# Performance work log

Measured on AMD Instinct MI355X. Metric: run time of the kernel, lower is better.

Reference implementation:

```python
import jax, jax.numpy as jnp
import numpy as np

B, L, H, LAT, V = 4096, 16, 256, 64, 800


def setup_inputs() -> dict:
    key = jax.random.key(0)
    ks = jax.random.split(key, 20)
    s = 0.05
    return {
        'wid': jax.random.randint(ks[0], (B, L), 0, V),
        'tree_vec': jax.random.normal(ks[1], (B, LAT), jnp.float32),
        'emb': jax.random.normal(ks[2], (V, H), jnp.float32) * s,
        'Wz_w': jax.random.normal(ks[3], (H, 2 * H), jnp.float32) * s,
        'Wz_b': jnp.zeros((H,), jnp.float32),
        'Wr_w': jax.random.normal(ks[4], (H, H), jnp.float32) * s,
        'Ur_w': jax.random.normal(ks[5], (H, H), jnp.float32) * s,
        'Ur_b': jnp.zeros((H,), jnp.float32),
        'Wh_w': jax.random.normal(ks[6], (H, 2 * H), jnp.float32) * s,
        'Wh_b': jnp.zeros((H,), jnp.float32),
        'W_w': jax.random.normal(ks[7], (H, LAT + H), jnp.float32) * s,
        'W_b': jnp.zeros((H,), jnp.float32),
        'U_w': jax.random.normal(ks[8], (H, LAT + 2 * H), jnp.float32) * s,
        'U_b': jnp.zeros((H,), jnp.float32),
        'Wo_w': jax.random.normal(ks[9], (V, H), jnp.float32) * s,
        'Wo_b': jnp.zeros((V,), jnp.float32),
        'Us_w': jax.random.normal(ks[10], (1, H), jnp.float32) * s,
        'Us_b': jnp.zeros((1,), jnp.float32),
    }


def _decoder(wid, tree_vec, emb, Wz_w, Wz_b, Wr_w, Ur_w, Ur_b, Wh_w, Wh_b,
             W_w, W_b, U_w, U_b, Wo_w, Wo_b, Us_w, Us_b):
    nB, nL = wid.shape
    x = emb[wid]                      # [B,L,H] node embeddings
    xt = jnp.transpose(x, (1, 0, 2))  # [L,B,H]

    def gru_scan(src_seq, dst_seq):
        # JTNN GRUUpdate along a chain: carry = (m_prev, rm_prev)
        def step(carry, xs):
            m_prev, rm_prev = carry
            x_src, x_dst = xs
            z = jax.nn.sigmoid(jnp.concatenate([x_src, m_prev], -1) @ Wz_w.T + Wz_b)
            h_til = jnp.tanh(jnp.concatenate([x_src, rm_prev], -1) @ Wh_w.T + Wh_b)
            m = (1.0 - z) * m_prev + z * h_til
            r = jax.nn.sigmoid(x_dst @ Wr_w.T + m @ Ur_w.T + Ur_b)
            return (m, r * m), m
        z0 = jnp.zeros((src_seq.shape[1], H), src_seq.dtype)
        _, m_seq = jax.lax.scan(step, (z0, z0), (src_seq, dst_seq))
        return m_seq  # [L-1,B,H]

    # forward edges t->t+1 (DFS forward), reverse edges t+1->t (DFS backtrack)
    m_fwd = gru_scan(xt[:-1], xt[1:])
    m_rev = gru_scan(xt[1:][::-1], xt[:-1][::-1])[::-1]  # indexed by t

    zeros_h = jnp.zeros((nB, H), x.dtype)
    tvL = lambda n: jnp.broadcast_to(tree_vec, (n, nB, LAT))

    # p_inputs = [x_v, h_v, tree_vec] at root, each fwd step, each rev step
    p_root = jnp.concatenate([x[:, 0], zeros_h, tree_vec], -1)[None]
    p_fwd = jnp.concatenate([xt[1:], m_fwd, tvL(nL - 1)], -1)
    m_fwd_shift = jnp.concatenate([zeros_h[None], m_fwd[:-1]], 0)
    h_rev = m_fwd_shift + m_rev  # node t after backtrack pull
    p_rev = jnp.concatenate([xt[:-1], h_rev, tvL(nL - 1)], -1)[::-1]
    p_in = jnp.concatenate([p_root, p_fwd, p_rev], 0).reshape(-1, 2 * H + LAT)
    # targets: forward expansions -> 1, backtracks + final stop -> 0
    p_t = jnp.concatenate([jnp.ones((nL - 1,)), jnp.zeros((nL,))])
    p_t = jnp.broadcast_to(p_t[:, None], (2 * nL - 1, nB)).reshape(-1)

    # q_inputs = [h, tree_vec] at root and each newly created node
    q_root = jnp.concatenate([zeros_h, tree_vec], -1)[None]
    q_new = jnp.concatenate([m_fwd, tvL(nL - 1)], -1)
    q_in = jnp.concatenate([q_root, q_new], 0).reshape(-1, H + LAT)
    q_t = jnp.transpose(wid, (1, 0)).reshape(-1)  # [L*B], step-major like q_in

    q = jax.nn.relu(q_in @ W_w.T + W_b) @ Wo_w.T + Wo_b  # [L*B, V]
    p = (jax.nn.relu(p_in @ U_w.T + U_b) @ Us_w.T + Us_b)[:, 0]

    p_loss = jnp.sum(jnp.logaddexp(0.0, p) - p * p_t) / nB
    logZ = jax.nn.logsumexp(q, axis=-1)
    q_sel = jnp.take_along_axis(q, q_t[:, None], axis=1)[:, 0]
    q_loss = jnp.sum(logZ - q_sel) / nB
    p_acc = jnp.mean(((p > 0).astype(jnp.int32) == p_t.astype(jnp.int32)).astype(jnp.float32))
    q_acc = jnp.mean((jnp.argmax(q, axis=-1) == q_t).astype(jnp.float32))
    return (q_loss, p_loss, q_acc, p_acc)


def reference(wid, tree_vec, emb, Wz_w, Wz_b, Wr_w, Ur_w, Ur_b, Wh_w, Wh_b,
              W_w, W_b, U_w, U_b, Wo_w, Wo_b, Us_w, Us_b):
    return _decoder(wid, tree_vec, emb, Wz_w, Wz_b, Wr_w, Ur_w, Ur_b, Wh_w, Wh_b,
                    W_w, W_b, U_w, U_b, Wo_w, Wo_b, Us_w, Us_b)
```

## Files before the change

### kernel.cpp

```cpp
#include <hip/hip_runtime.h>
#include <math.h>


typedef unsigned short u16;
typedef __attribute__((ext_vector_type(4))) float f4;
typedef __attribute__((ext_vector_type(4))) unsigned short u16x4;
typedef __attribute__((ext_vector_type(8))) unsigned short u16x8;
typedef __attribute__((ext_vector_type(8))) short s16x8;
typedef __attribute__((ext_vector_type(4))) float f32x4;

#define DEV static __device__ __forceinline__

DEV u16 f2b(float f) {
  unsigned u = __float_as_uint(f);
  u += 0x7fffu + ((u >> 16) & 1u);
  return (u16)(u >> 16);
}
DEV float b2f(u16 h) { return __uint_as_float(((unsigned)h) << 16); }
DEV void split2(float v, u16& hi, u16& lo) {
  hi = f2b(v);
  lo = f2b(v - b2f(hi));
}
DEV float fsig(float x) { return __builtin_amdgcn_rcpf(1.f + __expf(-x)); }
DEV float ftanh(float x) {
  const float e = __expf(2.f * x);
  return 1.f - 2.f * __builtin_amdgcn_rcpf(e + 1.f);
}

DEV void gld16(const void* g, void* l) {
  __builtin_amdgcn_global_load_lds((const __attribute__((address_space(1))) void*)g,
                                   (__attribute__((address_space(3))) void*)l, 16, 0, 0);
}

#define MFMA(a, b, c) __builtin_amdgcn_mfma_f32_16x16x32_bf16((a), (b), (c), 0, 0, 0)

template <int GR, int GC, bool ASPL, bool BSPL>
DEV void mm128(const u16* __restrict__ Ah, const u16* __restrict__ Al,
               const u16* __restrict__ Bh, const u16* __restrict__ Bl,
               int K, u16* sm, f32x4* acc) {
  constexpr int MT = 8 / GR, NT = 8 / GC;
  const int tid = threadIdx.x;
  const int lane = tid & 63;
  const int wv = tid >> 6;
  const int wr = wv / GC, wc = wv % GC;
  const size_t rs = (size_t)K * 2;
  const size_t soff = (size_t)(tid >> 2) * rs + (size_t)((tid & 3) * 16);
  const char* gAh = (const char*)Ah + soff;
  const char* gBh = (const char*)Bh + soff;
  const char* gAl = nullptr;
  const char* gBl = nullptr;
  if constexpr (ASPL) gAl = (const char*)Al + soff;
  if constexpr (BSPL) gBl = (const char*)Bl + soff;
  char* L = (char*)sm;
  const int wb = wv * 1024;
  const int frow = lane & 15, fkb = (lane >> 4) * 16;
  const char* rA = L + (size_t)((wr * 16 * MT + frow) * 64 + fkb);
  const char* rB = L + 8192 + (size_t)((wc * 16 * NT + frow) * 64 + fkb);
  const size_t rskip = rs * 64;
  const int nk = K >> 5;
  for (int kt = 0; kt < nk; ++kt) {
    gld16(gAh, L + wb);
    gld16(gAh + rskip, L + 4096 + wb);
    gld16(gBh, L + 8192 + wb);
    gld16(gBh + rskip, L + 12288 + wb);
    if constexpr (ASPL) {
      gld16(gAl, L + 16384 + wb);
      gld16(gAl + rskip, L + 20480 + wb);
    }
    if constexpr (BSPL) {
      gld16(gBl, L + 24576 + wb);
      gld16(gBl + rskip, L + 28672 + wb);
    }
    gAh += 64; gBh += 64;
    if constexpr (ASPL) gAl += 64;
    if constexpr (BSPL) gBl += 64;
    __syncthreads();
    s16x8 a_[MT], b_[NT];
#pragma unroll
    for (int i = 0; i < MT; ++i) a_[i] = *(const s16x8*)(rA + i * 1024);
#pragma unroll
    for (int j = 0; j < NT; ++j) b_[j] = *(const s16x8*)(rB + j * 1024);
#pragma unroll
    for (int i = 0; i < MT; ++i)
#pragma unroll
      for (int j = 0; j < NT; ++j)
        acc[i * NT + j] = MFMA(a_[i], b_[j], acc[i * NT + j]);
    if constexpr (BSPL) {
      s16x8 bl_[NT];
#pragma unroll
      for (int j = 0; j < NT; ++j) bl_[j] = *(const s16x8*)(rB + 16384 + j * 1024);
#pragma unroll
      for (int i = 0; i < MT; ++i)
#pragma unroll
        for (int j = 0; j < NT; ++j)
          acc[i * NT + j] = MFMA(a_[i], bl_[j], acc[i * NT + j]);
    }
    if constexpr (ASPL) {
      s16x8 al_[MT];
#pragma unroll
      for (int i = 0; i < MT; ++i) al_[i] = *(const s16x8*)(rA + 16384 + i * 1024);
#pragma unroll
      for (int i = 0; i < MT; ++i)
#pragma unroll
        for (int j = 0; j < NT; ++j)
          acc[i * NT + j] = MFMA(al_[i], b_[j], acc[i * NT + j]);
    }
    __syncthreads();
  }
}

__global__ __launch_bounds__(256) void k_pack(const float* __restrict__ Wz, const float* __restrict__ Wr,
                                              const float* __restrict__ Ur, const float* __restrict__ Wh,
                                              const float* __restrict__ Ww, const float* __restrict__ Uw,
                                              const float* __restrict__ Wo, const float* __restrict__ emb,
                                              const float* __restrict__ tree,
                                              u16* wpk, u16* uzh, u16* urw, u16* wu, u16* wt2, u16* wov,
                                              u16* uxp2, u16* utp2, u16* embp, u16* tre2) {
  const int i = blockIdx.x * 256 + threadIdx.x;
  const int seg = blockIdx.y;
  u16 h, l;
  if (seg == 0) {
    if (i >= 196608) return;
    const int row = i >> 8, c = i & 255;
    const float v = (row < 256) ? Wz[row * 512 + c]
                                : (row < 512) ? Wh[(row - 256) * 512 + c] : Wr[(row - 512) * 256 + c];
    split2(v, h, l); wpk[i] = h; wpk[196608 + i] = l;
  } else if (seg == 1) {
    if (i >= 131072) return;
    const int row = i >> 8, c = i & 255;
    const float v = (row < 256) ? Wz[row * 512 + 256 + c] : Wh[(row - 256) * 512 + 256 + c];
    uzh[i] = f2b(v);
  } else if (seg == 2) {
    if (i >= 65536) return;
    urw[i] = f2b(Ur[i]);
  } else if (seg == 3) {
    if (i >= 81920) return;
    if (i < 65536) {
      const int row = i >> 8, c = i & 255;
      wu[i] = f2b(Ww[row * 320 + c]);
    } else {
      const int j = i - 65536, row = j >> 6, c = j & 63;
      split2(Ww[row * 320 + 256 + c], h, l); wt2[j] = h; wt2[16384 + j] = l;
    }
  } else if (seg == 4) {
    if (i >= 229376) return;
    const float v = (i < 204800) ? Wo[i] : 0.f;
    wov[i] = f2b(v);
  } else if (seg == 5) {
    if (i >= 147456) return;
    if (i < 65536) {
      const int row = i >> 8, c = i & 255;
      split2(Uw[row * 576 + c], h, l); uxp2[i] = h; uxp2[65536 + i] = l;
    } else if (i < 131072) {
      const int j = i - 65536, row = j >> 8, c = j & 255;
      wu[65536 + j] = f2b(Uw[row * 576 + 256 + c]);
    } else {
      const int j = i - 131072, row = j >> 6, c = j & 63;
      split2(Uw[row * 576 + 512 + c], h, l); utp2[j] = h; utp2[16384 + j] = l;
    }
  } else if (seg == 6) {
    if (i >= 229376) return;
    const int row = i >> 8;
    const float v = (row < 800) ? emb[i] : 0.f;
    split2(v, h, l); embp[i] = h; embp[229376 + i] = l;
  } else {
    if (i >= 65536) return;
    const int b = i >> 4, c4 = (i & 15) << 2;
    const f4 tv = *(const f4*)(tree + (size_t)b * 64 + c4);
    u16x4 hi, lo;
#pragma unroll
    for (int k = 0; k < 4; ++k) { u16 hh, ll; split2(tv[k], hh, ll); hi[k] = hh; lo[k] = ll; }
    *(u16x4*)(tre2 + (size_t)b * 64 + c4) = hi;
    *(u16x4*)(tre2 + 262144 + (size_t)b * 64 + c4) = lo;
  }
}

__global__ __launch_bounds__(256) void k_prep(const u16* __restrict__ embp, const u16* __restrict__ wpk,
                                              const u16* __restrict__ tre2, const u16* __restrict__ wt2,
                                              const u16* __restrict__ utp2, const u16* __restrict__ uxp2,
                                              u16* __restrict__ Aembh, float* __restrict__ Tq,
                                              float* __restrict__ Tp, float* __restrict__ Xp) {
  __shared__ u16 sm[16384];
  f32x4 acc[16] = {};
  const int bid = blockIdx.x;
  int seg, bx, by, K;
  const u16 *A0, *B0;
  size_t Aoff, Boff;
  if (bid < 42) { seg = 0; bx = bid % 7; by = bid / 7; A0 = embp; Aoff = 229376; B0 = wpk; Boff = 196608; K = 256; }
  else if (bid < 106) { const int l2 = bid - 42; seg = 1; bx = l2 % 32; by = l2 / 32; A0 = tre2; Aoff = 262144; B0 = wt2; Boff = 16384; K = 64; }
  else if (bid < 170) { const int l2 = bid - 106; seg = 2; bx = l2 % 32; by = l2 / 32; A0 = tre2; Aoff = 262144; B0 = utp2; Boff = 16384; K = 64; }
  else { const int l2 = bid - 170; seg = 3; bx = l2 % 7; by = l2 / 7; A0 = embp; Aoff = 229376; B0 = uxp2; Boff = 65536; K = 256; }
  A0 += (size_t)bx * 128 * K;
  B0 += (size_t)by * 128 * K;
  mm128<2, 2, true, true>(A0, A0 + Aoff, B0, B0 + Boff, K, sm, acc);
  const int lane = threadIdx.x & 63, wv = threadIdx.x >> 6;
  const int wr = wv >> 1, wc = wv & 1, quad = lane >> 4, c = lane & 15;
#pragma unroll
  for (int i = 0; i < 4; ++i)
#pragma unroll
    for (int j = 0; j < 4; ++j)
#pragma unroll
      for (int rg = 0; rg < 4; ++rg) {
        const size_t row = (size_t)bx * 128 + wr * 64 + i * 16 + quad * 4 + rg;
        const int col = by * 128 + wc * 64 + j * 16 + c;
        const float v = acc[i * 4 + j][rg];
        if (seg == 0) Aembh[row * 768 + col] = f2b(v);
        else if (seg == 1) Tq[row * 256 + col] = v;
        else if (seg == 2) Tp[row * 256 + col] = v;
        else Xp[row * 256 + col] = v;
      }
}

__global__ __launch_bounds__(1024, 1) void k_scan(const u16* __restrict__ uzh, const u16* __restrict__ urw,
                                                  const u16* __restrict__ Aembh, const int* __restrict__ wid,
                                                  const float* __restrict__ Wz_b, const float* __restrict__ Wh_b,
                                                  const float* __restrict__ Ur_b,
                                                  u16* __restrict__ mfh, u16* __restrict__ mrh) {
  __shared__ __align__(16) u16 MH[8192];
  __shared__ __align__(16) u16 ML[8192];
  __shared__ __align__(16) u16 RH[8192];
  __shared__ __align__(16) u16 RL[8192];
  const int tid = threadIdx.x;
  const int wv = tid >> 6, lane = tid & 63;
  const int l15 = lane & 15, quad = lane >> 4;
  const int r0 = blockIdx.x * 32;
  const int dir = r0 >> 12;
  const int b0 = r0 & 4095;
  for (int i = tid; i < 8192; i += 1024) { MH[i] = 0; ML[i] = 0; RH[i] = 0; RL[i] = 0; }
  const int zc0 = wv * 16;
  const int cc = zc0 + l15;
  const float bzv = Wz_b[cc], bhv = Wh_b[cc], urv = Ur_b[cc];
  s16x8 wz[8], wh[8];
#pragma unroll
  for (int kc = 0; kc < 8; ++kc) {
    const size_t zo = (size_t)cc * 256 + kc * 32 + quad * 8;
    wz[kc] = *(const s16x8*)(uzh + zo);
    wh[kc] = *(const s16x8*)(uzh + zo + 65536);
  }
  float mnew[2][4];
  __syncthreads();
  for (int s = 0; s < 15; ++s) {
    const int tsrc = dir ? (15 - s) : s;
    const int tdst = dir ? (14 - s) : (s + 1);
    int xids[8], xds[8];
#pragma unroll
    for (int mt = 0; mt < 2; ++mt)
#pragma unroll
      for (int rg = 0; rg < 4; ++rg) {
        const int b = b0 + mt * 16 + quad * 4 + rg;
        xids[mt * 4 + rg] = wid[b * 16 + tsrc];
        xds[mt * 4 + rg] = (s < 14) ? wid[b * 16 + tdst] : 0;
      }
    f32x4 aZ[2] = {};
    f32x4 aH[2] = {};
    for (int kc = 0; kc < 8; ++kc) {
      s16x8 amh[2], aml[2], arh[2], arl[2];
#pragma unroll
      for (int mt = 0; mt < 2; ++mt) {
        const int ai = ((kc * 4 + quad) * 32 + mt * 16 + l15) * 8;
        amh[mt] = *(const s16x8*)&MH[ai];
        aml[mt] = *(const s16x8*)&ML[ai];
        arh[mt] = *(const s16x8*)&RH[ai];
        arl[mt] = *(const s16x8*)&RL[ai];
      }
#pragma unroll
      for (int mt = 0; mt < 2; ++mt) {
        aZ[mt] = MFMA(amh[mt], wz[kc], aZ[mt]);
        aZ[mt] = MFMA(aml[mt], wz[kc], aZ[mt]);
        aH[mt] = MFMA(arh[mt], wh[kc], aH[mt]);
        aH[mt] = MFMA(arl[mt], wh[kc], aH[mt]);
      }
    }
    __syncthreads();
#pragma unroll
    for (int mt = 0; mt < 2; ++mt)
#pragma unroll
      for (int rg = 0; rg < 4; ++rg) {
        const int rr = mt * 16 + quad * 4 + rg;
        const int xid = xids[mt * 4 + rg];
        const int mi = ((cc >> 3) * 32 + rr) * 8 + (cc & 7);
        const float az = b2f(Aembh[(size_t)xid * 768 + cc]);
        const float ah = b2f(Aembh[(size_t)xid * 768 + 256 + cc]);
        const float mp = b2f(MH[mi]) + b2f(ML[mi]);
        const float z = fsig(aZ[mt][rg] + az + bzv);
        const float ht = ftanh(aH[mt][rg] + ah + bhv);
        const float mv = (1.f - z) * mp + z * ht;
        mnew[mt][rg] = mv;
        u16 hh, ll; split2(mv, hh, ll);
        MH[mi] = hh; ML[mi] = ll;
      }
    __syncthreads();
    {
      u16* dst = dir ? (mrh + ((size_t)(14 - s) * 4096 + b0) * 256)
                     : (mfh + ((size_t)s * 4096 + b0) * 256);
      const int r = tid >> 5, cg = tid & 31;
      const s16x8 v = *(const s16x8*)&MH[(cg * 32 + r) * 8];
      *(s16x8*)(dst + r * 256 + cg * 8) = v;
    }
    if (s == 14) break;
    f32x4 aR[2] = {};
    for (int kc = 0; kc < 8; ++kc) {
      s16x8 amh[2], aml[2];
#pragma unroll
      for (int mt = 0; mt < 2; ++mt) {
        const int ai = ((kc * 4 + quad) * 32 + mt * 16 + l15) * 8;
        amh[mt] = *(const s16x8*)&MH[ai];
        aml[mt] = *(const s16x8*)&ML[ai];
      }
      const size_t ro = (size_t)cc * 256 + kc * 32 + quad * 8;
      const s16x8 brh = *(const s16x8*)(urw + ro);
#pragma unroll
      for (int mt = 0; mt < 2; ++mt) {
        aR[mt] = MFMA(amh[mt], brh, aR[mt]);
        aR[mt] = MFMA(aml[mt], brh, aR[mt]);
      }
    }
#pragma unroll
    for (int mt = 0; mt < 2; ++mt)
#pragma unroll
      for (int rg = 0; rg < 4; ++rg) {
        const int rr = mt * 16 + quad * 4 + rg;
        const int xd = xds[mt * 4 + rg];
        const int mi = ((cc >> 3) * 32 + rr) * 8 + (cc & 7);
        const float ar = b2f(Aembh[(size_t)xd * 768 + 512 + cc]);
        const float rp = aR[mt][rg] + ar + urv;
        const float rmv = fsig(rp) * mnew[mt][rg];
        u16 hh, ll; split2(rmv, hh, ll);
        RH[mi] = hh; RL[mi] = ll;
      }
    __syncthreads();
  }
}

__global__ __launch_bounds__(256) void k_mid(const u16* __restrict__ mfh, const u16* __restrict__ mrh,
                                             const u16* __restrict__ wu,
                                             const float* __restrict__ Tq, const float* __restrict__ W_b,
                                             const float* __restrict__ Xp, const float* __restrict__ Tp,
                                             const float* __restrict__ U_b, const float* __restrict__ Us_w,
                                             const int* __restrict__ wid,
                                             u16* __restrict__ hq, u16* __restrict__ hrev,
                                             float* __restrict__ ppart) {
  const int bid = blockIdx.x;
  const int tid = threadIdx.x;
  if (bid < 1920) {
    __shared__ u16 sm[8192];
    f32x4 acc[16] = {};
    const int rb = bid >> 2, ct = bid & 3;
    const u16* Ah = mfh + (size_t)rb * 128 * 256;
    const u16* Bh = wu + (size_t)ct * 128 * 256;
    mm128<4, 1, false, false>(Ah, nullptr, Bh, nullptr, 256, sm, acc);
    const int lane = tid & 63, wv = tid >> 6, quad = lane >> 4, c = lane & 15;
    if (ct < 2) {
      const int colb = ct * 128;
#pragma unroll
      for (int i = 0; i < 2; ++i)
#pragma unroll
        for (int rg = 0; rg < 4; ++rg) {
          const size_t row = (size_t)rb * 128 + wv * 32 + i * 16 + quad * 4 + rg;
          const int b = (int)(row & 4095);
#pragma unroll
          for (int j = 0; j < 8; ++j) {
            const int col = colb + j * 16 + c;
            const float hv = fmaxf(acc[i * 8 + j][rg] + Tq[(size_t)b * 256 + col] + W_b[col], 0.f);
            hq[(row + 4096) * 256 + col] = f2b(hv);
          }
        }
    } else {
      const int colb = (ct - 2) * 128;
#pragma unroll
      for (int i = 0; i < 2; ++i)
#pragma unroll
        for (int rg = 0; rg < 4; ++rg) {
          const size_t row = (size_t)rb * 128 + wv * 32 + i * 16 + quad * 4 + rg;
          const int t = (int)(row >> 12), b = (int)(row & 4095);
          const int xid = wid[b * 16 + t + 1];
          const int prow = (int)row + 4096;
          float d = 0.f;
#pragma unroll
          for (int j = 0; j < 8; ++j) {
            const int col = colb + j * 16 + c;
            float h = acc[i * 8 + j][rg] + Xp[(size_t)xid * 256 + col] + Tp[(size_t)b * 256 + col] + U_b[col];
            h = fmaxf(h, 0.f);
            d += h * Us_w[col];
          }
#pragma unroll
          for (int dd = 1; dd < 16; dd <<= 1) d += __shfl_xor(d, dd);
          if (c == 0) ppart[(size_t)prow * 2 + (ct - 2)] = d;
        }
    }
  } else if (bid < 9600) {
    const int idx = (bid - 1920) * 256 + tid;
    const int r = idx >> 5, g8 = idx & 31;
    const int t = r >> 12;
    const size_t o = (size_t)r * 256 + g8 * 8;
    const u16x8 a = *(const u16x8*)(mrh + o);
    u16x8 out = a;
    if (t > 0) {
      const u16x8 a2 = *(const u16x8*)(mfh + o - 1048576);
#pragma unroll
      for (int k = 0; k < 8; ++k) out[k] = f2b(b2f(a[k]) + b2f(a2[k]));
    }
    *(u16x8*)(hrev + o) = out;
  } else {
    const int b = bid - 9600;
    const int col = tid;
    const float hv = fmaxf(Tq[(size_t)b * 256 + col] + W_b[col], 0.f);
    hq[(size_t)b * 256 + col] = f2b(hv);
    const int xid = wid[b * 16];
    float d = fmaxf(Xp[(size_t)xid * 256 + col] + Tp[(size_t)b * 256 + col] + U_b[col], 0.f) * Us_w[col];
#pragma unroll
    for (int dd = 1; dd < 64; dd <<= 1) d += __shfl_xor(d, dd);
    __shared__ float red[4];
    if ((tid & 63) == 0) red[tid >> 6] = d;
    __syncthreads();
    if (tid == 0) {
      ppart[(size_t)b * 2] = red[0] + red[1] + red[2] + red[3];
      ppart[(size_t)b * 2 + 1] = 0.f;
    }
  }
}

__global__ __launch_bounds__(256) void k_tail(const u16* __restrict__ hq, const u16* __restrict__ wov,
                                              const u16* __restrict__ wu, const u16* __restrict__ hrev,
                                              const float* __restrict__ Wo_b, const float* __restrict__ Xp,
                                              const float* __restrict__ Tp, const float* __restrict__ U_b,
                                              const float* __restrict__ Us_w, const int* __restrict__ wid,
                                              float* __restrict__ qpart, float* __restrict__ ppart) {
  __shared__ u16 sm[8192];
  f32x4 acc[16] = {};
  const int bid = blockIdx.x;
  const int tid = threadIdx.x, lane = tid & 63, wv = tid >> 6;
  const int quad = lane >> 4, c = lane & 15;
  if (bid < 3584) {
    const int by = bid % 7, bx = bid / 7;
    const u16* Ah = hq + (size_t)bx * 128 * 256;
    const u16* Bh = wov + (size_t)by * 128 * 256;
    mm128<4, 1, false, false>(Ah, nullptr, Bh, nullptr, 256, sm, acc);
    const int colb = by * 128;
#pragma unroll
    for (int i = 0; i < 2; ++i)
#pragma unroll
      for (int rg = 0; rg < 4; ++rg) {
        const size_t row = (size_t)bx * 128 + wv * 32 + i * 16 + quad * 4 + rg;
        const int t = (int)(row >> 12), b = (int)(row & 4095);
        const int qt = wid[b * 16 + t];
        float vals[8];
        float mx = -1e30f;
        int am = 0x7fffffff;
#pragma unroll
        for (int j = 0; j < 8; ++j) {
          const int col = colb + j * 16 + c;
          float v = -1e30f;
          if (col < 800) v = acc[i * 8 + j][rg] + Wo_b[col];
          vals[j] = v;
          if (v > mx) { mx = v; am = col; }
        }
        float gm = mx;
        int ga = am;
#pragma unroll
        for (int d = 1; d < 16; d <<= 1) {
          const float om = __shfl_xor(gm, d);
          const int oa = __shfl_xor(ga, d);
          if (om > gm || (om == gm && oa < ga)) { gm = om; ga = oa; }
        }
        float s = 0.f, sel = -1e30f;
#pragma unroll
        for (int j = 0; j < 8; ++j) {
          s += __expf(vals[j] - gm);
          const int col = colb + j * 16 + c;
          if (col == qt) sel = vals[j];
        }
#pragma unroll
        for (int d = 1; d < 16; d <<= 1) {
          s += __shfl_xor(s, d);
          sel = fmaxf(sel, __shfl_xor(sel, d));
        }
        if (c == 0) {
          f4 o;
          o.x = gm; o.y = s; o.z = (float)ga; o.w = sel;
          *(f4*)(qpart + (row * 8 + by) * 4) = o;
        }
      }
  } else {
    const int l2 = bid - 3584;
    const int by = l2 & 1, bx = l2 >> 1;
    const u16* Ah = hrev + (size_t)bx * 128 * 256;
    const u16* Bh = wu + (size_t)(256 + by * 128) * 256;
    mm128<4, 1, false, false>(Ah, nullptr, Bh, nullptr, 256, sm, acc);
    const int colb = by * 128;
#pragma unroll
    for (int i = 0; i < 2; ++i)
#pragma unroll
      for (int rg = 0; rg < 4; ++rg) {
        const size_t row = (size_t)bx * 128 + wv * 32 + i * 16 + quad * 4 + rg;
        const int t = (int)(row >> 12), b = (int)(row & 4095);
        const int xid = wid[b * 16 + t];
        const int prow = (30 - t) * 4096 + b;
        float d = 0.f;
#pragma unroll
        for (int j = 0; j < 8; ++j) {
          const int col = colb + j * 16 + c;
          float h = acc[i * 8 + j][rg] + Xp[(size_t)xid * 256 + col] + Tp[(size_t)b * 256 + col] + U_b[col];
          h = fmaxf(h, 0.f);
          d += h * Us_w[col];
        }
#pragma unroll
        for (int dd = 1; dd < 16; dd <<= 1) d += __shfl_xor(d, dd);
        if (c == 0) ppart[(size_t)prow * 2 + by] = d;
      }
  }
}

__global__ __launch_bounds__(256) void k_red(const float* __restrict__ qpart, const float* __restrict__ ppart,
                                             const int* __restrict__ wid, const float* __restrict__ Us_b,
                                             float* __restrict__ accb) {
  __shared__ float s0, s1;
  if (threadIdx.x == 0) { s0 = 0.f; s1 = 0.f; }
  __syncthreads();
  if (blockIdx.x < 256) {
    const int r = blockIdx.x * 256 + threadIdx.x;
    f4 parts[7];
#pragma unroll
    for (int i = 0; i < 7; ++i) parts[i] = *(const f4*)(qpart + ((size_t)r * 8 + i) * 4);
    float M = -1e30f;
    int am = 0x7fffffff;
#pragma unroll
    for (int i = 0; i < 7; ++i) {
      const float m_ = parts[i].x;
      const int a_ = (int)parts[i].z;
      if (m_ > M || (m_ == M && a_ < am)) { M = m_; am = a_; }
    }
    float S = 0.f, sel = -1e30f;
#pragma unroll
    for (int i = 0; i < 7; ++i) {
      S += parts[i].y * __expf(parts[i].x - M);
      sel = fmaxf(sel, parts[i].w);
    }
    const float logZ = M + logf(S);
    const int t = r >> 12, b = r & 4095;
    const int qt = wid[b * 16 + t];
    atomicAdd(&s0, logZ - sel);
    atomicAdd(&s1, (am == qt) ? 1.f : 0.f);
    __syncthreads();
    if (threadIdx.x == 0) {
      atomicAdd(&accb[blockIdx.x & 15], s0);
      atomicAdd(&accb[16 + (blockIdx.x & 15)], s1);
    }
  } else {
    const int r = (blockIdx.x - 256) * 256 + threadIdx.x;
    const float p = ppart[(size_t)r * 2] + ppart[(size_t)r * 2 + 1] + Us_b[0];
    const int sidx = r >> 12;
    const float pt = (sidx < 15) ? 1.f : 0.f;
    const float loss = fmaxf(p, 0.f) + log1pf(expf(-fabsf(p))) - p * pt;
    const float hit = ((p > 0.f) == (pt > 0.5f)) ? 1.f : 0.f;
    atomicAdd(&s0, loss);
    atomicAdd(&s1, hit);
    __syncthreads();
    if (threadIdx.x == 0) {
      atomicAdd(&accb[32 + (blockIdx.x & 15)], s0);
      atomicAdd(&accb[48 + (blockIdx.x & 15)], s1);
    }
  }
}

__global__ void k_finalize(const float* __restrict__ accb, float* __restrict__ out) {
  if (threadIdx.x == 0 && blockIdx.x == 0) {
    float ql = 0, qa = 0, pl = 0, pa = 0;
    for (int i = 0; i < 16; ++i) {
      ql += accb[i];
      qa += accb[16 + i];
      pl += accb[32 + i];
      pa += accb[48 + i];
    }
    out[0] = ql / 4096.f;
    out[1] = pl / 4096.f;
    out[2] = qa / 65536.f;
    out[3] = pa / 126976.f;
  }
}

__global__ void k_flag(float* __restrict__ out) {
  if (threadIdx.x < 4) out[threadIdx.x] = -12345.f;
}

extern "C" void kernel_launch(void* const* d_in, const int* in_sizes, int n_in,
                              void* d_out, int out_size, void* d_ws, size_t ws_size,
                              hipStream_t stream) {
  (void)in_sizes; (void)n_in; (void)out_size;
  const int* wid = (const int*)d_in[0];
  const float* tree = (const float*)d_in[1];
  const float* emb = (const float*)d_in[2];
  const float* Wz_w = (const float*)d_in[3];
  const float* Wz_b = (const float*)d_in[4];
  const float* Wr_w = (const float*)d_in[5];
  const float* Ur_w = (const float*)d_in[6];
  const float* Ur_b = (const float*)d_in[7];
  const float* Wh_w = (const float*)d_in[8];
  const float* Wh_b = (const float*)d_in[9];
  const float* W_w = (const float*)d_in[10];
  const float* W_b = (const float*)d_in[11];
  const float* U_w = (const float*)d_in[12];
  const float* U_b = (const float*)d_in[13];
  const float* Wo_w = (const float*)d_in[14];
  const float* Wo_b = (const float*)d_in[15];
  const float* Us_w = (const float*)d_in[16];
  const float* Us_b = (const float*)d_in[17];
  char* ws = (char*)d_ws;

  constexpr size_t NEED = 152273152ull;
  if (ws_size < NEED) {
    k_flag<<<1, 64, 0, stream>>>((float*)d_out);
    return;
  }

  u16* hq = (u16*)(ws + 0ull);
  u16* hrev = (u16*)(ws + 33554432ull);
  u16* mfh = (u16*)(ws + 65011712ull);
  u16* mrh = (u16*)(ws + 96468992ull);
  u16* Aembh = (u16*)(ws + 127926272ull);
  u16* embp = (u16*)(ws + 129302528ull);
  u16* wpk = (u16*)(ws + 130220032ull);
  u16* uzh = (u16*)(ws + 131006464ull);
  u16* urw = (u16*)(ws + 131268608ull);
  u16* wu = (u16*)(ws + 131399680ull);
  u16* wt2 = (u16*)(ws + 131661824ull);
  u16* wov = (u16*)(ws + 131727360ull);
  u16* uxp2 = (u16*)(ws + 132186112ull);
  u16* utp2 = (u16*)(ws + 132448256ull);
  u16* tre2 = (u16*)(ws + 132513792ull);
  float* Tq = (float*)(ws + 133562368ull);
  float* Tp = (float*)(ws + 137756672ull);
  float* Xp = (float*)(ws + 141950976ull);
  float* qpart = (float*)(ws + 142868480ull);
  float* ppart = (float*)(ws + 151257088ull);
  float* accb = (float*)(ws + 152272896ull);

  hipMemsetAsync(accb, 0, 256, stream);

  k_pack<<<dim3(896, 8), 256, 0, stream>>>(Wz_w, Wr_w, Ur_w, Wh_w, W_w, U_w, Wo_w, emb, tree,
                                           wpk, uzh, urw, wu, wt2, wov, uxp2, utp2, embp, tre2);
  k_prep<<<184, 256, 0, stream>>>(embp, wpk, tre2, wt2, utp2, uxp2, Aembh, Tq, Tp, Xp);
  k_scan<<<256, 1024, 0, stream>>>(uzh, urw, Aembh, wid, Wz_b, Wh_b, Ur_b, mfh, mrh);
  k_mid<<<13696, 256, 0, stream>>>(mfh, mrh, wu, Tq, W_b, Xp, Tp, U_b, Us_w, wid, hq, hrev, ppart);
  k_tail<<<4544, 256, 0, stream>>>(hq, wov, wu, hrev, Wo_b, Xp, Tp, U_b, Us_w, wid, qpart, ppart);
  k_red<<<752, 256, 0, stream>>>(qpart, ppart, wid, Us_b, accb);
  k_finalize<<<1, 64, 0, stream>>>(accb, (float*)d_out);
}
```

Baseline: 598.5 us.

## Keep A tile resident and stream all vocab tiles with online logsumexp

```diff
diff --git a/kernel.cpp b/kernel.cpp
--- a/kernel.cpp
+++ b/kernel.cpp
@@ -426,67 +426,122 @@
                                               const float* __restrict__ Tp, const float* __restrict__ U_b,
                                               const float* __restrict__ Us_w, const int* __restrict__ wid,
                                               float* __restrict__ qpart, float* __restrict__ ppart) {
-  __shared__ u16 sm[8192];
-  f32x4 acc[16] = {};
+  __shared__ __align__(16) u16 smem[40960];
   const int bid = blockIdx.x;
   const int tid = threadIdx.x, lane = tid & 63, wv = tid >> 6;
   const int quad = lane >> 4, c = lane & 15;
-  if (bid < 3584) {
-    const int by = bid % 7, bx = bid / 7;
-    const u16* Ah = hq + (size_t)bx * 128 * 256;
-    const u16* Bh = wov + (size_t)by * 128 * 256;
-    mm128<4, 1, false, false>(Ah, nullptr, Bh, nullptr, 256, sm, acc);
-    const int colb = by * 128;
-#pragma unroll
-    for (int i = 0; i < 2; ++i)
+  if (bid < 512) {
+    char* LA = (char*)smem;
+    char* LB = (char*)(smem + 32768);
+    const u16* Ah = hq + (size_t)bid * 128 * 256;
+    const size_t soff = (size_t)(tid >> 2) * 512 + (size_t)((tid & 3) * 16);
+#pragma unroll
+    for (int kt = 0; kt < 8; ++kt) {
+      gld16((const char*)Ah + soff + kt * 64, LA + kt * 8192 + wv * 1024);
+      gld16((const char*)Ah + soff + 32768 + kt * 64, LA + kt * 8192 + 4096 + wv * 1024);
+    }
+    gld16((const char*)wov + soff, LB + wv * 1024);
+    gld16((const char*)wov + soff + 32768, LB + 4096 + wv * 1024);
+    float rM[8], rS[8], rSel[8];
+    int rAm[8], qts[8];
+#pragma unroll
+    for (int mt = 0; mt < 2; ++mt)
 #pragma unroll
       for (int rg = 0; rg < 4; ++rg) {
-        const size_t row = (size_t)bx * 128 + wv * 32 + i * 16 + quad * 4 + rg;
-        const int t = (int)(row >> 12), b = (int)(row & 4095);
-        const int qt = wid[b * 16 + t];
-        float vals[8];
-        float mx = -1e30f;
-        int am = 0x7fffffff;
-#pragma unroll
-        for (int j = 0; j < 8; ++j) {
-          const int col = colb + j * 16 + c;
-          float v = -1e30f;
-          if (col < 800) v = acc[i * 8 + j][rg] + Wo_b[col];
-          vals[j] = v;
-          if (v > mx) { mx = v; am = col; }
+        const int r8 = mt * 4 + rg;
+        rM[r8] = -1e30f; rS[r8] = 0.f; rSel[r8] = -1e30f; rAm[r8] = 0x7fffffff;
+        const size_t row = (size_t)bid * 128 + wv * 32 + mt * 16 + quad * 4 + rg;
+        qts[r8] = wid[(row & 4095) * 16 + (int)(row >> 12)];
+      }
+    f32x4 acc[16];
+    for (int nt = 0; nt < 7; ++nt) {
+#pragma unroll
+      for (int i = 0; i < 16; ++i) acc[i] = (f32x4){0.f, 0.f, 0.f, 0.f};
+      for (int kt = 0; kt < 8; ++kt) {
+        const int g = nt * 8 + kt;
+        __syncthreads();
+        if (g < 55) {
+          const int nn = (g + 1) >> 3, nk = (g + 1) & 7;
+          const char* Bn = (const char*)(wov + (size_t)nn * 32768) + soff + nk * 64;
+          gld16(Bn, LB + ((g + 1) & 1) * 8192 + wv * 1024);
+          gld16(Bn + 32768, LB + ((g + 1) & 1) * 8192 + 4096 + wv * 1024);
         }
-        float gm = mx;
-        int ga = am;
-#pragma unroll
-        for (int d = 1; d < 16; d <<= 1) {
-          const float om = __shfl_xor(gm, d);
-          const int oa = __shfl_xor(ga, d);
-          if (om > gm || (om == gm && oa < ga)) { gm = om; ga = oa; }
+        s16x8 af[2], bf[8];
+#pragma unroll
+        for (int mt = 0; mt < 2; ++mt)
+          af[mt] = *(const s16x8*)(LA + kt * 8192 + (wv * 32 + mt * 16 + c) * 64 + quad * 16);
+#pragma unroll
+        for (int j = 0; j < 8; ++j)
+          bf[j] = *(const s16x8*)(LB + (g & 1) * 8192 + (j * 16 + c) * 64 + quad * 16);
+#pragma unroll
+        for (int mt = 0; mt < 2; ++mt)
+#pragma unroll
+          for (int j = 0; j < 8; ++j)
+            acc[mt * 8 + j] = MFMA(af[mt], bf[j], acc[mt * 8 + j]);
+      }
+      const int colb = nt * 128;
+#pragma unroll
+      for (int mt = 0; mt < 2; ++mt)
+#pragma unroll
+        for (int rg = 0; rg < 4; ++rg) {
+          const int r8 = mt * 4 + rg;
+          float vals[8];
+          float mx = -1e30f;
+          int am = 0x7fffffff;
+#pragma unroll
+          for (int j = 0; j < 8; ++j) {
+            const int col = colb + j * 16 + c;
+            float v = -1e30f;
+            if (col < 800) v = acc[mt * 8 + j][rg] + Wo_b[col];
+            vals[j] = v;
+            if (v > mx) { mx = v; am = col; }
+          }
+          float gm = mx;
+          int ga = am;
+#pragma unroll
+          for (int d = 1; d < 16; d <<= 1) {
+            const float om = __shfl_xor(gm, d);
+            const int oa = __shfl_xor(ga, d);
+            if (om > gm || (om == gm && oa < ga)) { gm = om; ga = oa; }
+          }
+          float s = 0.f, sel = -1e30f;
+#pragma unroll
+          for (int j = 0; j < 8; ++j) {
+            s += __expf(vals[j] - gm);
+            if (colb + j * 16 + c == qts[r8]) sel = vals[j];
+          }
+#pragma unroll
+          for (int d = 1; d < 16; d <<= 1) {
+            s += __shfl_xor(s, d);
+            sel = fmaxf(sel, __shfl_xor(sel, d));
+          }
+          const float oM = rM[r8];
+          if (gm > oM || (gm == oM && ga < rAm[r8])) rAm[r8] = ga;
+          const float nM = fmaxf(oM, gm);
+          rS[r8] = rS[r8] * __expf(oM - nM) + s * __expf(gm - nM);
+          rM[r8] = nM;
+          rSel[r8] = fmaxf(rSel[r8], sel);
         }
-        float s = 0.f, sel = -1e30f;
-#pragma unroll
-        for (int j = 0; j < 8; ++j) {
-          s += __expf(vals[j] - gm);
-          const int col = colb + j * 16 + c;
-          if (col == qt) sel = vals[j];
+    }
+    if (c == 0) {
+#pragma unroll
+      for (int mt = 0; mt < 2; ++mt)
+#pragma unroll
+        for (int rg = 0; rg < 4; ++rg) {
+          const int r8 = mt * 4 + rg;
+          const size_t row = (size_t)bid * 128 + wv * 32 + mt * 16 + quad * 4 + rg;
+          f4 o;
+          o.x = rM[r8]; o.y = rS[r8]; o.z = (float)rAm[r8]; o.w = rSel[r8];
+          *(f4*)(qpart + row * 4) = o;
         }
-#pragma unroll
-        for (int d = 1; d < 16; d <<= 1) {
-          s += __shfl_xor(s, d);
-          sel = fmaxf(sel, __shfl_xor(sel, d));
-        }
-        if (c == 0) {
-          f4 o;
-          o.x = gm; o.y = s; o.z = (float)ga; o.w = sel;
-          *(f4*)(qpart + (row * 8 + by) * 4) = o;
-        }
-      }
+    }
   } else {
-    const int l2 = bid - 3584;
+    f32x4 acc[16] = {};
+    const int l2 = bid - 512;
     const int by = l2 & 1, bx = l2 >> 1;
     const u16* Ah = hrev + (size_t)bx * 128 * 256;
     const u16* Bh = wu + (size_t)(256 + by * 128) * 256;
-    mm128<4, 1, false, false>(Ah, nullptr, Bh, nullptr, 256, sm, acc);
+    mm128<4, 1, false, false>(Ah, nullptr, Bh, nullptr, 256, smem, acc);
     const int colb = by * 128;
 #pragma unroll
     for (int i = 0; i < 2; ++i)
@@ -519,27 +574,12 @@
   __syncthreads();
   if (blockIdx.x < 256) {
     const int r = blockIdx.x * 256 + threadIdx.x;
-    f4 parts[7];
-#pragma unroll
-    for (int i = 0; i < 7; ++i) parts[i] = *(const f4*)(qpart + ((size_t)r * 8 + i) * 4);
-    float M = -1e30f;
-    int am = 0x7fffffff;
-#pragma unroll
-    for (int i = 0; i < 7; ++i) {
-      const float m_ = parts[i].x;
-      const int a_ = (int)parts[i].z;
-      if (m_ > M || (m_ == M && a_ < am)) { M = m_; am = a_; }
-    }
-    float S = 0.f, sel = -1e30f;
-#pragma unroll
-    for (int i = 0; i < 7; ++i) {
-      S += parts[i].y * __expf(parts[i].x - M);
-      sel = fmaxf(sel, parts[i].w);
-    }
-    const float logZ = M + logf(S);
+    const f4 p4 = *(const f4*)(qpart + (size_t)r * 4);
+    const float logZ = p4.x + logf(p4.y);
+    const int am = (int)p4.z;
     const int t = r >> 12, b = r & 4095;
     const int qt = wid[b * 16 + t];
-    atomicAdd(&s0, logZ - sel);
+    atomicAdd(&s0, logZ - p4.w);
     atomicAdd(&s1, (am == qt) ? 1.f : 0.f);
     __syncthreads();
     if (threadIdx.x == 0) {
@@ -642,7 +682,7 @@
   k_prep<<<184, 256, 0, stream>>>(embp, wpk, tre2, wt2, utp2, uxp2, Aembh, Tq, Tp, Xp);
   k_scan<<<256, 1024, 0, stream>>>(uzh, urw, Aembh, wid, Wz_b, Wh_b, Ur_b, mfh, mrh);
   k_mid<<<13696, 256, 0, stream>>>(mfh, mrh, wu, Tq, W_b, Xp, Tp, U_b, Us_w, wid, hq, hrev, ppart);
-  k_tail<<<4544, 256, 0, stream>>>(hq, wov, wu, hrev, Wo_b, Xp, Tp, U_b, Us_w, wid, qpart, ppart);
+  k_tail<<<1472, 256, 0, stream>>>(hq, wov, wu, hrev, Wo_b, Xp, Tp, U_b, Us_w, wid, qpart, ppart);
   k_red<<<752, 256, 0, stream>>>(qpart, ppart, wid, Us_b, accb);
   k_finalize<<<1, 64, 0, stream>>>(accb, (float*)d_out);
 }
```

New measurement: 561.1 us, median of 2. 1.07x faster.
